# Performance work log

Hardware: AMD Instinct MI355X
Metric: run time of the kernel (lower is better)

Reference implementation:

```python
import jax, jax.numpy as jnp
import numpy as np

HEADS = 8  # from init_kwargs

def setup_inputs() -> dict:
    key = jax.random.key(0)
    ks = jax.random.split(key, 9)
    N, S, E = 8, 2048, 512
    scale = 1.0 / np.sqrt(E)
    return {
        "values": jax.random.normal(ks[0], (N, S, E), jnp.float32),
        "keys": jax.random.normal(ks[1], (N, S, E), jnp.float32),
        "query": jax.random.normal(ks[2], (N, S, E), jnp.float32),
        "mask": jnp.ones((N, 1, 1, S), jnp.int32),
        "Wv": jax.random.normal(ks[3], (E, E), jnp.float32) * scale,
        "Wk": jax.random.normal(ks[4], (E, E), jnp.float32) * scale,
        "Wq": jax.random.normal(ks[5], (E, E), jnp.float32) * scale,
        "Wo": jax.random.normal(ks[6], (E, E), jnp.float32) * scale,
        "bo": jnp.zeros((E,), jnp.float32),
    }

def reference(values, keys, query, mask, Wv, Wk, Wq, Wo, bo):
    N, Q, E = query.shape
    H = HEADS
    D = E // H
    v = (values @ Wv).reshape(N, -1, H, D)  # [N,K,H,D]
    k = (keys @ Wk).reshape(N, -1, H, D)
    q = (query @ Wq).reshape(N, Q, H, D)
    energy = jnp.einsum('nqhd,nkhd->nhqk', q, k)  # [N,H,Q,K]
    energy = jnp.where(mask == 0, jnp.float32(-1e20), energy)
    attn = jax.nn.softmax(energy / jnp.sqrt(jnp.float32(D)), axis=3)
    out = jnp.einsum('nhqk,nkhd->nqhd', attn, v).reshape(N, Q, E)
    return out @ Wo + bo
```

## Files before the change

### kernel.cpp

```cpp
#include <hip/hip_runtime.h>
#include <hip/hip_bf16.h>
#include <stdint.h>

typedef __bf16 bf16;
typedef __bf16 bf16x8 __attribute__((ext_vector_type(8)));
typedef __bf16 bf16x4v __attribute__((ext_vector_type(4)));
typedef float  f32x4  __attribute__((ext_vector_type(4)));
typedef float  f32x16 __attribute__((ext_vector_type(16)));
typedef unsigned int u32x4 __attribute__((ext_vector_type(4)));

#define NB    8
#define SEQ   2048
#define EMB   512
#define NHEAD 8
#define HD    64

static __device__ __forceinline__ f32x4 mfma16(bf16x8 a, bf16x8 b, f32x4 c) {
    return __builtin_amdgcn_mfma_f32_16x16x32_bf16(a, b, c, 0, 0, 0);
}
static __device__ __forceinline__ f32x16 mfma32(bf16x8 a, bf16x8 b, f32x16 c) {
    return __builtin_amdgcn_mfma_f32_32x32x16_bf16(a, b, c, 0, 0, 0);
}
static __device__ __forceinline__ float ex2(float x) {
    float r; asm("v_exp_f32 %0, %1" : "=v"(r) : "v"(x)); return r;
}
static __device__ __forceinline__ unsigned pkbf(float lo, float hi) {
    unsigned d; asm("v_cvt_pk_bf16_f32 %0, %1, %2" : "=v"(d) : "v"(lo), "v"(hi)); return d;
}
static __device__ __forceinline__ void gload_lds16(const void* g, void* l) {
    __builtin_amdgcn_global_load_lds(
        (const __attribute__((address_space(1))) unsigned int*)g,
        (__attribute__((address_space(3))) unsigned int*)l, 16, 0, 0);
}
#define PRIO1 __builtin_amdgcn_s_setprio(1)
#define PRIO0 __builtin_amdgcn_s_setprio(0)

__global__ __launch_bounds__(256) void prep_weights(
    const float* __restrict__ Wv, const float* __restrict__ Wk,
    const float* __restrict__ Wq, const float* __restrict__ Wo,
    bf16* __restrict__ wt)
{
    int idx = blockIdx.x * 256 + threadIdx.x;
    int w   = idx >> 18;
    int rem = idx & 262143;
    int k   = rem >> 9;
    int n   = rem & 511;
    const float* src = (w == 0) ? Wv : (w == 1) ? Wk : (w == 2) ? Wq : Wo;
    wt[(size_t)w * 262144 + (size_t)n * 512 + k] = (bf16)src[k * 512 + n];
}

template <bool A_F32, bool FINAL>
__global__ __launch_bounds__(256) void gemm_kernel(
    const void* __restrict__ Ap, const bf16* __restrict__ Bt,
    void* __restrict__ Cp, const float* __restrict__ bias, float oscale)
{
    __shared__ __align__(16) bf16 As[128][72];
    __shared__ __align__(16) bf16 Bs[128][72];

    const int t    = threadIdx.x;
    const int lane = t & 63;
    const int wave = t >> 6;
    const int wr   = wave >> 1, wc = wave & 1;
    const int l15  = lane & 15, lg = lane >> 4;
    const long row0 = (long)blockIdx.x * 128;
    const int  col0 = blockIdx.y * 128;

    f32x4 acc[4][4];
#pragma unroll
    for (int i = 0; i < 4; i++)
#pragma unroll
        for (int j = 0; j < 4; j++) acc[i][j] = (f32x4){0.f, 0.f, 0.f, 0.f};

    for (int k0 = 0; k0 < 512; k0 += 64) {
        __syncthreads();
        if (A_F32) {
            const float* A = (const float*)Ap;
#pragma unroll
            for (int i = 0; i < 8; i++) {
                int c  = t + 256 * i;
                int r  = c >> 4;
                int cc = (c & 15) * 4;
                f32x4 v = *(const f32x4*)(A + (row0 + r) * 512 + k0 + cc);
                bf16x4v pk = { (bf16)v[0], (bf16)v[1], (bf16)v[2], (bf16)v[3] };
                *(bf16x4v*)&As[r][cc] = pk;
            }
        } else {
            const bf16* A = (const bf16*)Ap;
#pragma unroll
            for (int i = 0; i < 4; i++) {
                int c  = t + 256 * i;
                int r  = c >> 3;
                int cc = (c & 7) * 8;
                *(bf16x8*)&As[r][cc] = *(const bf16x8*)(A + (row0 + r) * 512 + k0 + cc);
            }
        }
#pragma unroll
        for (int i = 0; i < 4; i++) {
            int c  = t + 256 * i;
            int r  = c >> 3;
            int cc = (c & 7) * 8;
            *(bf16x8*)&Bs[r][cc] = *(const bf16x8*)(Bt + (size_t)(col0 + r) * 512 + k0 + cc);
        }
        __syncthreads();
#pragma unroll
        for (int kc = 0; kc < 64; kc += 32) {
            bf16x8 af[4], bfv[4];
#pragma unroll
            for (int mb = 0; mb < 4; mb++)
                af[mb] = *(bf16x8*)&As[wr * 64 + mb * 16 + l15][kc + lg * 8];
#pragma unroll
            for (int nb = 0; nb < 4; nb++)
                bfv[nb] = *(bf16x8*)&Bs[wc * 64 + nb * 16 + l15][kc + lg * 8];
#pragma unroll
            for (int mb = 0; mb < 4; mb++)
#pragma unroll
                for (int nb = 0; nb < 4; nb++)
                    acc[mb][nb] = mfma16(af[mb], bfv[nb], acc[mb][nb]);
        }
    }

#pragma unroll
    for (int mb = 0; mb < 4; mb++)
#pragma unroll
        for (int nb = 0; nb < 4; nb++)
#pragma unroll
            for (int r = 0; r < 4; r++) {
                long grow = row0 + wr * 64 + mb * 16 + lg * 4 + r;
                int  gcol = col0 + wc * 64 + nb * 16 + l15;
                float v = acc[mb][nb][r];
                if (FINAL) {
                    ((float*)Cp)[grow * 512 + gcol] = v + bias[gcol];
                } else {
                    ((bf16*)Cp)[grow * 512 + gcol] = (bf16)(v * oscale);
                }
            }
}

__global__ __launch_bounds__(512, 2) void attn_kernel(
    const bf16* __restrict__ Qg, const bf16* __restrict__ Kg,
    const bf16* __restrict__ Vg, const int* __restrict__ mask,
    bf16* __restrict__ ctx)
{
    __shared__ __align__(16) bf16 Ks[4][4096];
    __shared__ __align__(16) bf16 Vt[4][4096];
    __shared__ __align__(16) bf16 Ob[8][32 * 72];

    const int t    = threadIdx.x;
    const int lane = t & 63;
    const int w    = t >> 6;
    const int l31  = lane & 31;
    const int hi   = lane >> 5;
    const int h = blockIdx.x, n = blockIdx.y, qt = blockIdx.z;

    const size_t nbase   = (size_t)n * SEQ;
    const size_t headoff = (size_t)h * 64;
    const int q0 = qt * 512 + w * 64;

    const int k5_  = lane & 31;
    const int hi2_ = (k5_ >> 2) & 1;
    const int r_   = (k5_ & 3) + 4 * (k5_ >> 3);
    const int vpos = ((lane >> 5) * 2 + (r_ >> 3)) * 16 + hi2_ * 8 + (r_ & 7);

    int* mflags = (int*)&Ob[0][0];
    {
        const int* mp0 = mask + n * SEQ + t * 4;
        int mok = (mp0[0] != 0) & (mp0[1] != 0) & (mp0[2] != 0) & (mp0[3] != 0);
        unsigned long long b = __ballot(mok);
        if (lane == 0) mflags[w] = (b == ~0ULL) ? 1 : 0;
    }

    bf16x8 qf[2][4];
#pragma unroll
    for (int qb = 0; qb < 2; ++qb)
#pragma unroll
        for (int ds = 0; ds < 4; ++ds)
            qf[qb][ds] = *(const bf16x8*)(Qg + (nbase + q0 + qb * 32 + l31) * 512 + headoff + ds * 16 + hi * 8);

    f32x16 o[2][2] = {};
    float l_run[2] = {0.f, 0.f};

    const bf16* kg = Kg + (nbase + w * 8 + (lane >> 3)) * 512 + headoff + (((lane & 7) ^ (lane >> 3)) << 3);
    const bf16* vg = Vg + (nbase + lane) * 512 + headoff + w * 8;
    const int*  mp = mask + n * SEQ;

#define VSCAT(VR, VB) do {                                                    \
        char* vbp = (char*)(VB);                                              \
        _Pragma("unroll") for (int j = 0; j < 8; ++j)                         \
            *(bf16*)(vbp + (8 * w + j) * 128 + ((2 * vpos) ^ (j << 4))) = (VR)[j]; \
    } while (0)

    gload_lds16(kg,                     (char*)&Ks[0][0] + w * 1024);
    gload_lds16(kg + (size_t)64 * 512,  (char*)&Ks[1][0] + w * 1024);
    bf16x8 vrA = *(const bf16x8*)vg;
    bf16x8 vrB = *(const bf16x8*)(vg + (size_t)64 * 512);
    VSCAT(vrA, &Vt[0][0]);
    VSCAT(vrB, &Vt[1][0]);
    __syncthreads();
    const int maskall = mflags[0] & mflags[1] & mflags[2] & mflags[3] &
                        mflags[4] & mflags[5] & mflags[6] & mflags[7];

    f32x16 p[2][2];
    u32x4  bq[2][4];

#define QK_TILE(KB) do {                                                      \
        const char* kbb = (const char*)(KB);                                  \
        f32x16 zz = {};                                                       \
        p[0][0] = zz; p[0][1] = zz; p[1][0] = zz; p[1][1] = zz;               \
        PRIO1;                                                                \
        _Pragma("unroll")                                                     \
        for (int ds = 0; ds < 4; ++ds) {                                      \
            int sw = (ds * 32 + hi * 16) ^ ((l31 & 7) << 4);                  \
            bf16x8 kf0 = *(const bf16x8*)(kbb + l31 * 128 + sw);              \
            bf16x8 kf1 = *(const bf16x8*)(kbb + (32 + l31) * 128 + sw);       \
            p[0][0] = mfma32(kf0, qf[0][ds], p[0][0]);                        \
            p[1][0] = mfma32(kf0, qf[1][ds], p[1][0]);                        \
            p[0][1] = mfma32(kf1, qf[0][ds], p[0][1]);                        \
            p[1][1] = mfma32(kf1, qf[1][ds], p[1][1]);                        \
        }                                                                     \
        PRIO0;                                                                \
    } while (0)

#define MASK_TILE(T) do {                                                     \
        if (!maskall) {                                                       \
            int mv = mp[(T) * 64 + lane];                                     \
            unsigned long long mb = __ballot(mv != 0);                        \
            if (mb != ~0ULL) {                                                \
                _Pragma("unroll") for (int qb = 0; qb < 2; ++qb)              \
                _Pragma("unroll") for (int kb = 0; kb < 2; ++kb) {            \
                    float* pp = (float*)&p[qb][kb];                           \
                    _Pragma("unroll") for (int r = 0; r < 16; ++r) {          \
                        int kk = kb * 32 + (r & 3) + 8 * (r >> 2) + 4 * hi;   \
                        if (!((mb >> kk) & 1)) pp[r] = -1e30f;                \
                    }                                                         \
                }                                                             \
            }                                                                 \
        }                                                                     \
    } while (0)

#define SM_PACK do {                                                          \
        _Pragma("unroll")                                                     \
        for (int qb = 0; qb < 2; ++qb) {                                      \
            float* p0 = (float*)&p[qb][0];                                    \
            float* p1 = (float*)&p[qb][1];                                    \
            float sa0 = 0.f, sa1 = 0.f, sa2 = 0.f, sa3 = 0.f;                 \
            _Pragma("unroll") for (int r = 0; r < 16; r += 4) {               \
                float e0 = ex2(p0[r]);   p0[r]   = e0; sa0 += e0;             \
                float e1 = ex2(p0[r+1]); p0[r+1] = e1; sa1 += e1;             \
                float e2 = ex2(p0[r+2]); p0[r+2] = e2; sa2 += e2;             \
                float e3 = ex2(p0[r+3]); p0[r+3] = e3; sa3 += e3;             \
            }                                                                 \
            _Pragma("unroll") for (int r = 0; r < 16; r += 4) {               \
                float e0 = ex2(p1[r]);   p1[r]   = e0; sa0 += e0;             \
                float e1 = ex2(p1[r+1]); p1[r+1] = e1; sa1 += e1;             \
                float e2 = ex2(p1[r+2]); p1[r+2] = e2; sa2 += e2;             \
                float e3 = ex2(p1[r+3]); p1[r+3] = e3; sa3 += e3;             \
            }                                                                 \
            float sl = (sa0 + sa1) + (sa2 + sa3);                             \
            l_run[qb] += sl + __shfl_xor(sl, 32);                             \
            _Pragma("unroll")                                                 \
            for (int ks = 0; ks < 4; ++ks) {                                  \
                float* ps = (ks >> 1) ? p1 : p0;                              \
                int bo = (ks & 1) * 8;                                        \
                bq[qb][ks] = (u32x4){ pkbf(ps[bo + 0], ps[bo + 1]),           \
                                      pkbf(ps[bo + 2], ps[bo + 3]),           \
                                      pkbf(ps[bo + 4], ps[bo + 5]),           \
                                      pkbf(ps[bo + 6], ps[bo + 7]) };         \
            }                                                                 \
        }                                                                     \
    } while (0)

#define PV_TILE(VB) do {                                                      \
        const char* vbb = (const char*)(VB);                                  \
        PRIO1;                                                                \
        _Pragma("unroll")                                                     \
        for (int ks = 0; ks < 4; ++ks) {                                      \
            int sw = (ks * 32 + hi * 16) ^ ((l31 & 7) << 4);                  \
            bf16x8 vf0 = *(const bf16x8*)(vbb + l31 * 128 + sw);              \
            bf16x8 vf1 = *(const bf16x8*)(vbb + (32 + l31) * 128 + sw);       \
            union { u32x4 u; bf16x8 v; } c0, c1;                              \
            c0.u = bq[0][ks]; c1.u = bq[1][ks];                               \
            o[0][0] = mfma32(vf0, c0.v, o[0][0]);                             \
            o[0][1] = mfma32(vf0, c1.v, o[0][1]);                             \
            o[1][0] = mfma32(vf1, c0.v, o[1][0]);                             \
            o[1][1] = mfma32(vf1, c1.v, o[1][1]);                             \
        }                                                                     \
        PRIO0;                                                                \
    } while (0)

    for (int e = 0; e < 16; ++e) {
        const int bA = (e & 1) * 2, bB = bA + 1;
        const int nA = bA ^ 2,      nB = bB ^ 2;
        if (e < 15) {
            gload_lds16(kg + (size_t)(2 * e + 2) * 64 * 512, (char*)&Ks[nA][0] + w * 1024);
            gload_lds16(kg + (size_t)(2 * e + 3) * 64 * 512, (char*)&Ks[nB][0] + w * 1024);
            vrA = *(const bf16x8*)(vg + (size_t)(2 * e + 2) * 64 * 512);
            vrB = *(const bf16x8*)(vg + (size_t)(2 * e + 3) * 64 * 512);
        }
        QK_TILE(&Ks[bA][0]);
        MASK_TILE(2 * e);
        SM_PACK;
        PV_TILE(&Vt[bA][0]);
        QK_TILE(&Ks[bB][0]);
        MASK_TILE(2 * e + 1);
        SM_PACK;
        PV_TILE(&Vt[bB][0]);
        if (e < 15) {
            VSCAT(vrA, &Vt[nA][0]);
            VSCAT(vrB, &Vt[nB][0]);
        }
        __syncthreads();
    }

#pragma unroll
    for (int qb = 0; qb < 2; ++qb) {
        float inv = 1.f / l_run[qb];
        bf16* ob = &Ob[w][0];
#pragma unroll
        for (int db = 0; db < 2; ++db) {
            float* oo = (float*)&o[db][qb];
#pragma unroll
            for (int r = 0; r < 16; ++r) {
                int d = db * 32 + (r & 3) + 8 * (r >> 2) + 4 * hi;
                ob[l31 * 72 + d] = (bf16)(oo[r] * inv);
            }
        }
#pragma unroll
        for (int i = 0; i < 2; ++i)
#pragma unroll
            for (int half = 0; half < 2; ++half) {
                int ql = i * 16 + (lane >> 2);
                int d8 = (lane & 3) * 8 + half * 32;
                bf16x8 vv = *(const bf16x8*)(ob + ql * 72 + d8);
                *(bf16x8*)(ctx + (nbase + q0 + qb * 32 + ql) * 512 + headoff + d8) = vv;
            }
    }
#undef VSCAT
#undef QK_TILE
#undef MASK_TILE
#undef SM_PACK
#undef PV_TILE
}

extern "C" void kernel_launch(void* const* d_in, const int* in_sizes, int n_in,
                              void* d_out, int out_size, void* d_ws, size_t ws_size,
                              hipStream_t stream) {
    (void)in_sizes; (void)n_in; (void)out_size; (void)ws_size;
    const float* values = (const float*)d_in[0];
    const float* keys   = (const float*)d_in[1];
    const float* query  = (const float*)d_in[2];
    const int*   mask   = (const int*)d_in[3];
    const float* Wv = (const float*)d_in[4];
    const float* Wk = (const float*)d_in[5];
    const float* Wq = (const float*)d_in[6];
    const float* Wo = (const float*)d_in[7];
    const float* bo = (const float*)d_in[8];
    float* out = (float*)d_out;

    char* ws = (char*)d_ws;
    bf16* wt = (bf16*)(ws);
    bf16* Qb = (bf16*)(ws + ((size_t)2  << 20));
    bf16* Kb = (bf16*)(ws + ((size_t)18 << 20));
    bf16* Vb = (bf16*)(ws + ((size_t)34 << 20));
    bf16* Cb = (bf16*)(ws + ((size_t)50 << 20));

    const float SC = 0.18033688011f;

    prep_weights<<<4096, 256, 0, stream>>>(Wv, Wk, Wq, Wo, wt);
    gemm_kernel<true, false><<<dim3(128, 4), 256, 0, stream>>>(values, wt,              Vb, nullptr, 1.0f);
    gemm_kernel<true, false><<<dim3(128, 4), 256, 0, stream>>>(keys,   wt + 262144,     Kb, nullptr, 1.0f);
    gemm_kernel<true, false><<<dim3(128, 4), 256, 0, stream>>>(query,  wt + 2 * 262144, Qb, nullptr, SC);
    attn_kernel<<<dim3(8, 8, 4), 512, 0, stream>>>(Qb, Kb, Vb, mask, Cb);
    gemm_kernel<false, true><<<dim3(128, 4), 256, 0, stream>>>(Cb, wt + 3 * 262144, out, bo, 1.0f);
}
```

Measured before the change: 169.1 us.

## Tile weight transpose via LDS and use direct global-to-LDS loads in GEMM

The weight prep kernel now transposes 64x64 tiles through shared memory, so global reads and writes are coalesced instead of strided scatter writes. The GEMM loads bf16 operand tiles with global_load_lds straight into an XOR-swizzled LDS layout, which removes the register round-trip and the row padding while keeping LDS reads free of bank conflicts. The fp32 A path keeps the old padded layout in the same byte buffer. The swizzle indexing has to match between the writes and the reads, which adds risk of subtle layout errors.

```diff
diff --git a/kernel.cpp b/kernel.cpp
--- a/kernel.cpp
+++ b/kernel.cpp
@@ -40,13 +40,27 @@
     const float* __restrict__ Wq, const float* __restrict__ Wo,
     bf16* __restrict__ wt)
 {
-    int idx = blockIdx.x * 256 + threadIdx.x;
-    int w   = idx >> 18;
-    int rem = idx & 262143;
-    int k   = rem >> 9;
-    int n   = rem & 511;
-    const float* src = (w == 0) ? Wv : (w == 1) ? Wk : (w == 2) ? Wq : Wo;
-    wt[(size_t)w * 262144 + (size_t)n * 512 + k] = (bf16)src[k * 512 + n];
+    __shared__ float Ls[64][65];
+    const int b    = blockIdx.x;
+    const int wsel = b >> 6;
+    const int kt   = (b & 63) >> 3;
+    const int nt   = b & 7;
+    const int t    = threadIdx.x;
+    const float* src = (wsel == 0) ? Wv : (wsel == 1) ? Wk : (wsel == 2) ? Wq : Wo;
+
+#pragma unroll
+    for (int i = 0; i < 16; ++i) {
+        int e = i * 256 + t;
+        int k = e >> 6, n = e & 63;
+        Ls[k][n] = src[(size_t)(kt * 64 + k) * 512 + nt * 64 + n];
+    }
+    __syncthreads();
+#pragma unroll
+    for (int i = 0; i < 16; ++i) {
+        int e = i * 256 + t;
+        int n = e >> 6, k = e & 63;
+        wt[(size_t)wsel * 262144 + (size_t)(nt * 64 + n) * 512 + kt * 64 + k] = (bf16)Ls[k][n];
+    }
 }
 
 template <bool A_F32, bool FINAL>
@@ -54,8 +68,8 @@
     const void* __restrict__ Ap, const bf16* __restrict__ Bt,
     void* __restrict__ Cp, const float* __restrict__ bias, float oscale)
 {
-    __shared__ __align__(16) bf16 As[128][72];
-    __shared__ __align__(16) bf16 Bs[128][72];
+    __shared__ __align__(16) char AsM[128 * 144];
+    __shared__ __align__(16) bf16 Bs[128][64];
 
     const int t    = threadIdx.x;
     const int lane = t & 63;
@@ -82,35 +96,44 @@
                 int cc = (c & 15) * 4;
                 f32x4 v = *(const f32x4*)(A + (row0 + r) * 512 + k0 + cc);
                 bf16x4v pk = { (bf16)v[0], (bf16)v[1], (bf16)v[2], (bf16)v[3] };
-                *(bf16x4v*)&As[r][cc] = pk;
+                *(bf16x4v*)(AsM + r * 144 + cc * 2) = pk;
             }
         } else {
             const bf16* A = (const bf16*)Ap;
 #pragma unroll
             for (int i = 0; i < 4; i++) {
-                int c  = t + 256 * i;
-                int r  = c >> 3;
-                int cc = (c & 7) * 8;
-                *(bf16x8*)&As[r][cc] = *(const bf16x8*)(A + (row0 + r) * 512 + k0 + cc);
+                int chunk = i * 4 + wave;
+                int c = chunk * 64 + lane;
+                int r = c >> 3, u = c & 7;
+                gload_lds16(A + (row0 + r) * 512 + k0 + ((u ^ (r & 7)) << 3),
+                            AsM + chunk * 1024);
             }
         }
 #pragma unroll
         for (int i = 0; i < 4; i++) {
-            int c  = t + 256 * i;
-            int r  = c >> 3;
-            int cc = (c & 7) * 8;
-            *(bf16x8*)&Bs[r][cc] = *(const bf16x8*)(Bt + (size_t)(col0 + r) * 512 + k0 + cc);
+            int chunk = i * 4 + wave;
+            int c = chunk * 64 + lane;
+            int r = c >> 3, u = c & 7;
+            gload_lds16(Bt + (size_t)(col0 + r) * 512 + k0 + ((u ^ (r & 7)) << 3),
+                        (char*)&Bs[0][0] + chunk * 1024);
         }
         __syncthreads();
 #pragma unroll
         for (int kc = 0; kc < 64; kc += 32) {
             bf16x8 af[4], bfv[4];
 #pragma unroll
-            for (int mb = 0; mb < 4; mb++)
-                af[mb] = *(bf16x8*)&As[wr * 64 + mb * 16 + l15][kc + lg * 8];
-#pragma unroll
-            for (int nb = 0; nb < 4; nb++)
-                bfv[nb] = *(bf16x8*)&Bs[wc * 64 + nb * 16 + l15][kc + lg * 8];
+            for (int mb = 0; mb < 4; mb++) {
+                int row = wr * 64 + mb * 16 + l15;
+                if (A_F32)
+                    af[mb] = *(bf16x8*)(AsM + row * 144 + (kc + lg * 8) * 2);
+                else
+                    af[mb] = *(bf16x8*)(AsM + row * 128 + (((lg + (kc >> 3)) ^ (l15 & 7)) << 4));
+            }
+#pragma unroll
+            for (int nb = 0; nb < 4; nb++) {
+                int row = wc * 64 + nb * 16 + l15;
+                bfv[nb] = *(bf16x8*)((char*)&Bs[0][0] + row * 128 + (((lg + (kc >> 3)) ^ (l15 & 7)) << 4));
+            }
 #pragma unroll
             for (int mb = 0; mb < 4; mb++)
 #pragma unroll
@@ -365,7 +388,7 @@
 
     const float SC = 0.18033688011f;
 
-    prep_weights<<<4096, 256, 0, stream>>>(Wv, Wk, Wq, Wo, wt);
+    prep_weights<<<256, 256, 0, stream>>>(Wv, Wk, Wq, Wo, wt);
     gemm_kernel<true, false><<<dim3(128, 4), 256, 0, stream>>>(values, wt,              Vb, nullptr, 1.0f);
     gemm_kernel<true, false><<<dim3(128, 4), 256, 0, stream>>>(keys,   wt + 262144,     Kb, nullptr, 1.0f);
     gemm_kernel<true, false><<<dim3(128, 4), 256, 0, stream>>>(query,  wt + 2 * 262144, Qb, nullptr, SC);
```

New measurement: 162.3 us. 4.0% less time.
